# Kernel optimization log

Hardware: AMD Instinct MI355X
Metric: run time of the kernel (lower is better)

The kernel has to match this reference:

```python
import itertools
import jax, jax.numpy as jnp
import numpy as np

N_QUBITS = 8
N_LAYERS = 2
BATCH = 8192
INPUT_DIM = 3072
NUM_CLASSES = 10

_In = np.eye(2, dtype=np.complex64)
_Xn = np.array([[0, 1], [1, 0]], dtype=np.complex64)
_Yn = np.array([[0, -1j], [1j, 0]], dtype=np.complex64)
_Zn = np.array([[1, 0], [0, -1]], dtype=np.complex64)
_P = {"I": _In, "X": _Xn, "Y": _Yn, "Z": _Zn}
_XX = jnp.asarray(np.kron(_Xn, _Xn))
_YY = jnp.asarray(np.kron(_Yn, _Yn))
_ZZ = jnp.asarray(np.kron(_Zn, _Zn))
_I4 = jnp.eye(4, dtype=jnp.complex64)
# 2-qubit Pauli words in PennyLane ArbitraryUnitary order: IX, IY, IZ, XI, ..., ZZ
_WORDS = jnp.asarray(np.stack([np.kron(_P[a], _P[b]) for a, b in itertools.product("IXYZ", repeat=2)][1:]))


def apply_gate(state, U, wires):
    """Apply a 2^k x 2^k gate U to the given wires of a (2,)*n statevector."""
    n = state.ndim
    k = len(wires)
    U = U.reshape((2,) * (2 * k)).astype(state.dtype)
    state = jnp.tensordot(U, state, axes=(list(range(k, 2 * k)), list(wires)))
    rest = [a for a in range(n) if a not in wires]
    perm = [0] * n
    for i, a in enumerate(wires):
        perm[a] = i
    for j, a in enumerate(rest):
        perm[a] = k + j
    return jnp.transpose(state, perm)


def u3_mat(t, p, d):
    ct, st = jnp.cos(t / 2).astype(jnp.complex64), jnp.sin(t / 2).astype(jnp.complex64)
    r0 = jnp.stack([ct, -jnp.exp(1j * d) * st])
    r1 = jnp.stack([jnp.exp(1j * p) * st, jnp.exp(1j * (p + d)) * ct])
    return jnp.stack([r0, r1])


def ry_mat(t):
    c, s = jnp.cos(t / 2), jnp.sin(t / 2)
    return jnp.stack([jnp.stack([c, -s]), jnp.stack([s, c])]).astype(jnp.complex64)


def ising_mat(phi, pauli2):
    # exp(-i phi/2 P) for two-qubit Pauli word P (P^2 = I)
    return jnp.cos(phi / 2) * _I4 - 1j * jnp.sin(phi / 2) * pauli2


def circuit(conv_w, pool_w, last_w, feats):
    state = jnp.zeros((2,) * N_QUBITS, jnp.complex64).at[(0,) * N_QUBITS].set(1.0)
    # AngleEmbedding with RY rotations
    for w in range(N_QUBITS):
        state = apply_gate(state, ry_mat(feats[w]), (w,))
    wires = list(range(N_QUBITS))
    for layer in range(N_LAYERS):
        cw = conv_w[layer]
        nw = len(wires)
        for p in (0, 1):
            for idx in range(nw - 1):
                if idx % 2 == p:
                    a, b = wires[idx], wires[idx + 1]
                    state = apply_gate(state, u3_mat(cw[idx, 0], cw[idx, 1], cw[idx, 2]), (a,))
                    state = apply_gate(state, u3_mat(cw[idx + 1, 3], cw[idx + 1, 4], cw[idx + 1, 5]), (b,))
                    state = apply_gate(state, ising_mat(cw[idx, 6], _ZZ), (a, b))
                    state = apply_gate(state, ising_mat(cw[idx, 7], _YY), (a, b))
                    state = apply_gate(state, ising_mat(cw[idx, 8], _XX), (a, b))
                    state = apply_gate(state, u3_mat(cw[idx, 9], cw[idx, 10], cw[idx, 11]), (a,))
                    state = apply_gate(state, u3_mat(cw[idx + 1, 12], cw[idx + 1, 13], cw[idx + 1, 14]), (b,))
        # Pooling: mid-circuit measure + conditional U3 == (deferred measurement)
        pw = pool_w[layer]
        for idx in range(1, nw, 2):
            u = u3_mat(pw[idx // 2, 0], pw[idx // 2, 1], pw[idx // 2, 2])
            cu = jnp.zeros((4, 4), jnp.complex64).at[0, 0].set(1.0).at[1, 1].set(1.0).at[2:, 2:].set(u)
            state = apply_gate(state, cu, (wires[idx], wires[idx - 1]))
        wires = wires[::2]
    # ArbitraryUnitary on remaining 2 wires: product of 15 PauliRot gates
    for k in range(15):
        mat = jnp.cos(last_w[k] / 2) * _I4 - 1j * jnp.sin(last_w[k] / 2) * _WORDS[k]
        state = apply_gate(state, mat, tuple(wires))
    probs = state.real ** 2 + state.imag ** 2
    z = jnp.sum(probs, axis=tuple(range(1, N_QUBITS)))  # (2,)
    return z[0] - z[1]


def setup_inputs() -> dict:
    key = jax.random.key(0)
    ks = jax.random.split(key, 8)
    return {
        "x": jax.random.normal(ks[0], (BATCH, INPUT_DIM), jnp.float32),
        "fc_w": jax.random.normal(ks[1], (N_QUBITS, INPUT_DIM), jnp.float32) * 0.02,
        "fc_b": jnp.zeros((N_QUBITS,), jnp.float32),
        "conv_params": jax.random.normal(ks[2], (N_LAYERS, N_QUBITS, 15), jnp.float32),
        "pool_params": jax.random.normal(ks[3], (N_LAYERS, N_QUBITS // 2, 3), jnp.float32),
        "last_params": jax.random.normal(ks[4], (15,), jnp.float32),
        "out_w": jax.random.normal(ks[5], (NUM_CLASSES, 1), jnp.float32),
        "out_b": jnp.zeros((NUM_CLASSES,), jnp.float32),
    }


def reference(x, fc_w, fc_b, conv_params, pool_params, last_params, out_w, out_b):
    feats = jnp.tanh(x.reshape(x.shape[0], -1) @ fc_w.T + fc_b)  # (B, n_qubits)
    qvals = jax.vmap(lambda f: circuit(conv_params, pool_params, last_params, f))(feats)
    logits = qvals[:, None].astype(x.dtype) @ out_w.T + out_b  # (B, num_classes)
    return logits
```

## Files before the change

kernel.cpp:

```cpp
#include <hip/hip_runtime.h>
#include <math.h>

__constant__ int G_ORD[17] = {0,1,2,3,4,5,6, 10,11,12,13, 7,8,9, 14,15, 16};
__constant__ int G_WA[17]  = {0,2,4,6,1,3,5, 1,3,5,7, 0,4,2, 2,6, 0};
__constant__ int G_WB[17]  = {1,3,5,7,2,4,6, 0,2,4,6, 2,6,4, 0,4, 4};
__constant__ int CDESC[10][3] = {{0,0,1},{0,2,3},{0,4,5},{0,6,7},{0,1,2},{0,3,4},{0,5,6},
                                 {1,0,1},{1,2,3},{1,1,2}};
__constant__ int PDESC[6][2] = {{0,0},{0,1},{0,2},{0,3},{1,0},{1,1}};
__constant__ float2 PMAT[4][4] = {
  {{1.f,0.f},{0.f,0.f},{0.f,0.f},{1.f,0.f}},
  {{0.f,0.f},{1.f,0.f},{1.f,0.f},{0.f,0.f}},
  {{0.f,0.f},{0.f,-1.f},{0.f,1.f},{0.f,0.f}},
  {{1.f,0.f},{0.f,0.f},{0.f,0.f},{-1.f,0.f}}};

__device__ __forceinline__ float2 cmul(float2 a, float2 b){
  return make_float2(a.x*b.x - a.y*b.y, a.x*b.y + a.y*b.x);
}
__device__ __forceinline__ float2 cadd(float2 a, float2 b){
  return make_float2(a.x+b.x, a.y+b.y);
}

__device__ void u3m(float t, float p, float d, float2* u){
  float ct = cosf(0.5f*t), st = sinf(0.5f*t);
  u[0] = make_float2(ct, 0.f);
  u[1] = make_float2(-cosf(d)*st, -sinf(d)*st);
  u[2] = make_float2(cosf(p)*st,  sinf(p)*st);
  u[3] = make_float2(cosf(p+d)*ct, sinf(p+d)*ct);
}

__device__ void kron2(const float2* A, const float2* B, float2* M){
  #pragma unroll
  for (int ia=0; ia<2; ia++)
    #pragma unroll
    for (int ib=0; ib<2; ib++)
      #pragma unroll
      for (int ja=0; ja<2; ja++)
        #pragma unroll
        for (int jb=0; jb<2; jb++)
          M[(ia*2+ib)*4 + (ja*2+jb)] = cmul(A[ia*2+ja], B[ib*2+jb]);
}

__device__ void mul44(const float2* A, const float2* B, float2* C){
  #pragma unroll
  for (int r=0;r<4;r++)
    #pragma unroll
    for (int c=0;c<4;c++){
      float2 s = make_float2(0.f,0.f);
      #pragma unroll
      for (int k=0;k<4;k++) s = cadd(s, cmul(A[r*4+k], B[k*4+c]));
      C[r*4+c] = s;
    }
}

__device__ void rotword(float phi, int qa, int qb, float2* R){
  float ch = cosf(0.5f*phi), sh = sinf(0.5f*phi);
  float2 W[16];
  kron2(PMAT[qa], PMAT[qb], W);
  #pragma unroll
  for (int i=0;i<16;i++) R[i] = make_float2(sh*W[i].y, -sh*W[i].x);
  #pragma unroll
  for (int d=0;d<4;d++) R[d*4+d].x += ch;
}

__global__ __launch_bounds__(64) void build_gates_kernel(
    const float* __restrict__ conv, const float* __restrict__ pool,
    const float* __restrict__ last, float* __restrict__ gates){
  int t = threadIdx.x;
  float2 M[16], T[16], R[16];
  if (t < 10){
    int layer = CDESC[t][0], ra = CDESC[t][1], rb = CDESC[t][2];
    const float* cw = conv + layer*120;
    int bA = ra*15, bB = rb*15;
    float2 A1[4], B1[4], A2[4], B2[4], K[16];
    u3m(cw[bA+0], cw[bA+1], cw[bA+2], A1);
    u3m(cw[bB+3], cw[bB+4], cw[bB+5], B1);
    kron2(A1, B1, M);
    rotword(cw[bA+6], 3, 3, R); mul44(R, M, T);
    rotword(cw[bA+7], 2, 2, R); mul44(R, T, M);
    rotword(cw[bA+8], 1, 1, R); mul44(R, M, T);
    u3m(cw[bA+9],  cw[bA+10], cw[bA+11], A2);
    u3m(cw[bB+12], cw[bB+13], cw[bB+14], B2);
    kron2(A2, B2, K); mul44(K, T, M);
  } else if (t < 16){
    int layer = PDESC[t-10][0], h = PDESC[t-10][1];
    const float* pw = pool + layer*12 + h*3;
    float2 u[4];
    u3m(pw[0], pw[1], pw[2], u);
    #pragma unroll
    for (int i=0;i<16;i++) M[i] = make_float2(0.f,0.f);
    M[0]  = make_float2(1.f,0.f);
    M[5]  = make_float2(1.f,0.f);
    M[10] = u[0]; M[11] = u[1]; M[14] = u[2]; M[15] = u[3];
  } else if (t == 16){
    #pragma unroll
    for (int i=0;i<16;i++) M[i] = make_float2((i%5==0)?1.f:0.f, 0.f);
    for (int k=0;k<15;k++){
      int w = k+1;
      rotword(last[k], w>>2, w&3, R);
      mul44(R, M, T);
      #pragma unroll
      for (int i=0;i<16;i++) M[i] = T[i];
    }
  }
  if (t < 17){
    float2* dst = (float2*)(gates + t*32);
    #pragma unroll
    for (int i=0;i<16;i++) dst[i] = M[i];
  }
}

__global__ __launch_bounds__(64) void build_u_kernel(
    const float* __restrict__ gates, float2* __restrict__ U){
  __shared__ float2 st[256];
  int lane = threadIdx.x, col = blockIdx.x;
  #pragma unroll
  for (int k=lane; k<256; k+=64) st[k] = make_float2(k==col ? 1.f : 0.f, 0.f);
  __syncthreads();
  for (int g=0; g<17; g++){
    int slot = G_ORD[g];
    const float2* gm = (const float2*)(gates + slot*32);
    float2 m[16];
    #pragma unroll
    for (int i=0;i<16;i++) m[i] = gm[i];
    int pa = 7 - G_WA[g], pb = 7 - G_WB[g];
    int plo = pa < pb ? pa : pb, phi_ = pa < pb ? pb : pa;
    int mm = lane;
    int t1   = ((mm >> plo) << (plo+1)) | (mm & ((1<<plo)-1));
    int base = ((t1 >> phi_) << (phi_+1)) | (t1 & ((1<<phi_)-1));
    int ba = 1<<pa, bb = 1<<pb;
    int i0 = base, i1 = base|bb, i2 = base|ba, i3 = base|ba|bb;
    float2 s0 = st[i0], s1 = st[i1], s2 = st[i2], s3 = st[i3];
    float2 n0 = cadd(cadd(cmul(m[0], s0), cmul(m[1], s1)), cadd(cmul(m[2], s2), cmul(m[3], s3)));
    float2 n1 = cadd(cadd(cmul(m[4], s0), cmul(m[5], s1)), cadd(cmul(m[6], s2), cmul(m[7], s3)));
    float2 n2 = cadd(cadd(cmul(m[8], s0), cmul(m[9], s1)), cadd(cmul(m[10],s2), cmul(m[11],s3)));
    float2 n3 = cadd(cadd(cmul(m[12],s0), cmul(m[13],s1)), cadd(cmul(m[14],s2), cmul(m[15],s3)));
    st[i0] = n0; st[i1] = n1; st[i2] = n2; st[i3] = n3;
    __syncthreads();
  }
  #pragma unroll
  for (int k=lane; k<256; k+=64) U[k*256 + col] = st[k];
}

__global__ __launch_bounds__(256) void build_a_kernel(
    const float2* __restrict__ U, float* __restrict__ A){
  int j = threadIdx.x, i0 = blockIdx.x*2;
  float a0=0.f, a1=0.f;
  #pragma unroll 8
  for (int k=0; k<256; k++){
    float2 uj = U[k*256 + j];
    float2 u0 = U[k*256 + i0+0];
    float2 u1 = U[k*256 + i0+1];
    float sgn = (k < 128) ? 1.f : -1.f;
    a0 += sgn*(u0.x*uj.x + u0.y*uj.y);
    a1 += sgn*(u1.x*uj.x + u1.y*uj.y);
  }
  A[(i0+0)*256 + j] = a0;
  A[(i0+1)*256 + j] = a1;
}

__global__ __launch_bounds__(256) void feats_kernel(
    const float* __restrict__ x, const float* __restrict__ fcw,
    const float* __restrict__ fcb, float* __restrict__ feats){
  __shared__ float red[128*68];
  int t = threadIdx.x, lane = t & 63, wv = t >> 6;
  int r0 = blockIdx.x * 16;
  int rw = r0 + wv*4;
  const float4* x4 = (const float4*)x;
  const float4* w4 = (const float4*)fcw;
  float acc[4][8];
  #pragma unroll
  for (int r=0;r<4;r++)
    #pragma unroll
    for (int o=0;o<8;o++) acc[r][o] = 0.f;
  for (int p=0; p<12; p++){
    float4 wf[8];
    #pragma unroll
    for (int o=0;o<8;o++) wf[o] = w4[o*768 + p*64 + lane];
    #pragma unroll
    for (int r=0;r<4;r++){
      float4 xv = x4[(size_t)(rw+r)*768 + p*64 + lane];
      #pragma unroll
      for (int o=0;o<8;o++){
        acc[r][o] += xv.x*wf[o].x + xv.y*wf[o].y + xv.z*wf[o].z + xv.w*wf[o].w;
      }
    }
  }
  #pragma unroll
  for (int r=0;r<4;r++)
    #pragma unroll
    for (int o=0;o<8;o++)
      red[((wv*4+r)*8 + o)*68 + lane] = acc[r][o];
  __syncthreads();
  if (t < 128){
    const float4* rp = (const float4*)(red + t*68);
    float4 s4 = make_float4(0.f,0.f,0.f,0.f);
    #pragma unroll
    for (int i=0;i<16;i++){
      float4 v = rp[i];
      s4.x += v.x; s4.y += v.y; s4.z += v.z; s4.w += v.w;
    }
    float s = s4.x + s4.y + s4.z + s4.w + fcb[t & 7];
    feats[(r0 + (t>>3))*8 + (t&7)] = tanhf(s);
  }
}

__global__ __launch_bounds__(256) void qform_kernel(
    const float* __restrict__ Ag, const float* __restrict__ feats,
    const float* __restrict__ outw, const float* __restrict__ outb,
    float* __restrict__ out){
  __shared__ float As[32*256];
  __shared__ float ps[16*256];
  int t = threadIdx.x;
  int r0 = blockIdx.x * 16;
  {
    int row = t >> 4, i1 = t & 15;
    const float* f = feats + (r0 + row)*8;
    float c[8], s[8];
    #pragma unroll
    for (int w=0; w<8; w++){
      float a = 0.5f*f[w];
      __sincosf(a, &s[w], &c[w]);
    }
    float Hv = (i1&8 ? s[0]:c[0]) * (i1&4 ? s[1]:c[1])
             * (i1&2 ? s[2]:c[2]) * (i1&1 ? s[3]:c[3]);
    float l2[2], l4[4], l8[8], L[16];
    l2[0]=c[4]; l2[1]=s[4];
    #pragma unroll
    for (int a=0;a<2;a++){ l4[a*2]=l2[a]*c[5]; l4[a*2+1]=l2[a]*s[5]; }
    #pragma unroll
    for (int a=0;a<4;a++){ l8[a*2]=l4[a]*c[6]; l8[a*2+1]=l4[a]*s[6]; }
    #pragma unroll
    for (int a=0;a<8;a++){ L[a*2]=l8[a]*c[7]; L[a*2+1]=l8[a]*s[7]; }
    float* dst = ps + row*256 + i1*16;
    #pragma unroll
    for (int j=0;j<16;j++) dst[j] = Hv*L[j];
  }
  int wv = t >> 6, jb = t & 63;
  const float4* As4 = (const float4*)As;
  const float4* ps4 = (const float4*)ps;
  float4 acc4[4];
  #pragma unroll
  for (int r=0;r<4;r++) acc4[r] = make_float4(0.f,0.f,0.f,0.f);
  for (int chunk=0; chunk<8; chunk++){
    __syncthreads();
    #pragma unroll
    for (int pass=0; pass<8; pass++){
      int kk = pass*4 + wv;
      *(float4*)(As + kk*256 + jb*4) =
        *(const float4*)(Ag + (chunk*32 + kk)*256 + jb*4);
    }
    __syncthreads();
    #pragma unroll
    for (int kk4=0; kk4<8; kk4++){
      float4 av0 = As4[(kk4*4+0)*64 + jb];
      float4 av1 = As4[(kk4*4+1)*64 + jb];
      float4 av2 = As4[(kk4*4+2)*64 + jb];
      float4 av3 = As4[(kk4*4+3)*64 + jb];
      #pragma unroll
      for (int r=0; r<4; r++){
        float4 pv = ps4[(wv*4+r)*64 + chunk*8 + kk4];
        acc4[r].x += pv.x*av0.x + pv.y*av1.x + pv.z*av2.x + pv.w*av3.x;
        acc4[r].y += pv.x*av0.y + pv.y*av1.y + pv.z*av2.y + pv.w*av3.y;
        acc4[r].z += pv.x*av0.z + pv.y*av1.z + pv.z*av2.z + pv.w*av3.z;
        acc4[r].w += pv.x*av0.w + pv.y*av1.w + pv.z*av2.w + pv.w*av3.w;
      }
    }
  }
  float p[4];
  #pragma unroll
  for (int r=0; r<4; r++){
    float4 psv = ps4[(wv*4+r)*64 + jb];
    float pr = acc4[r].x*psv.x + acc4[r].y*psv.y + acc4[r].z*psv.z + acc4[r].w*psv.w;
    #pragma unroll
    for (int m=1; m<64; m<<=1) pr += __shfl_xor(pr, m, 64);
    p[r] = pr;
  }
  if (jb < 40){
    int ridx = jb / 10, c = jb - ridx*10;
    float q = (ridx==0) ? p[0] : (ridx==1) ? p[1] : (ridx==2) ? p[2] : p[3];
    out[(r0 + wv*4 + ridx)*10 + c] = q*outw[c] + outb[c];
  }
}

extern "C" void kernel_launch(void* const* d_in, const int* in_sizes, int n_in,
                              void* d_out, int out_size, void* d_ws, size_t ws_size,
                              hipStream_t stream) {
  const float* x    = (const float*)d_in[0];
  const float* fcw  = (const float*)d_in[1];
  const float* fcb  = (const float*)d_in[2];
  const float* conv = (const float*)d_in[3];
  const float* pool = (const float*)d_in[4];
  const float* last = (const float*)d_in[5];
  const float* outw = (const float*)d_in[6];
  const float* outb = (const float*)d_in[7];
  float* out = (float*)d_out;

  float* ws = (float*)d_ws;
  float*  gates = ws;
  float2* U     = (float2*)(ws + 1024);
  float*  Am    = ws + 1024 + 131072;
  float*  feats = Am + 65536;

  build_gates_kernel<<<1, 64, 0, stream>>>(conv, pool, last, gates);
  build_u_kernel<<<256, 64, 0, stream>>>(gates, U);
  build_a_kernel<<<128, 256, 0, stream>>>(U, Am);
  feats_kernel<<<512, 256, 0, stream>>>(x, fcw, fcb, feats);
  qform_kernel<<<512, 256, 0, stream>>>(Am, feats, outw, outb, out);
}
```

Baseline: 259.0 us.

## Fuse gate building into U kernel, split A rows, retile quadratic-form kernel

Gate matrix construction moves into every build_u block, held in shared memory, which removes one kernel launch and a global round trip, at the cost of redundant per-block gate computation. build_a now computes one row per block across twice as many blocks. The qform kernel drops to 128 threads, each holding 8 row accumulators, writes ps with float4 stores and stages its outputs through shared memory. Lower occupancy and higher register pressure in qform could offset the gains; the feats loop also gets an unroll hint.

```diff
diff --git a/kernel.cpp b/kernel.cpp
--- a/kernel.cpp
+++ b/kernel.cpp
@@ -62,69 +62,65 @@
   for (int d=0;d<4;d++) R[d*4+d].x += ch;
 }
 
-__global__ __launch_bounds__(64) void build_gates_kernel(
+__global__ __launch_bounds__(64) void build_u_kernel(
     const float* __restrict__ conv, const float* __restrict__ pool,
-    const float* __restrict__ last, float* __restrict__ gates){
-  int t = threadIdx.x;
-  float2 M[16], T[16], R[16];
-  if (t < 10){
-    int layer = CDESC[t][0], ra = CDESC[t][1], rb = CDESC[t][2];
-    const float* cw = conv + layer*120;
-    int bA = ra*15, bB = rb*15;
-    float2 A1[4], B1[4], A2[4], B2[4], K[16];
-    u3m(cw[bA+0], cw[bA+1], cw[bA+2], A1);
-    u3m(cw[bB+3], cw[bB+4], cw[bB+5], B1);
-    kron2(A1, B1, M);
-    rotword(cw[bA+6], 3, 3, R); mul44(R, M, T);
-    rotword(cw[bA+7], 2, 2, R); mul44(R, T, M);
-    rotword(cw[bA+8], 1, 1, R); mul44(R, M, T);
-    u3m(cw[bA+9],  cw[bA+10], cw[bA+11], A2);
-    u3m(cw[bB+12], cw[bB+13], cw[bB+14], B2);
-    kron2(A2, B2, K); mul44(K, T, M);
-  } else if (t < 16){
-    int layer = PDESC[t-10][0], h = PDESC[t-10][1];
-    const float* pw = pool + layer*12 + h*3;
-    float2 u[4];
-    u3m(pw[0], pw[1], pw[2], u);
-    #pragma unroll
-    for (int i=0;i<16;i++) M[i] = make_float2(0.f,0.f);
-    M[0]  = make_float2(1.f,0.f);
-    M[5]  = make_float2(1.f,0.f);
-    M[10] = u[0]; M[11] = u[1]; M[14] = u[2]; M[15] = u[3];
-  } else if (t == 16){
-    #pragma unroll
-    for (int i=0;i<16;i++) M[i] = make_float2((i%5==0)?1.f:0.f, 0.f);
-    for (int k=0;k<15;k++){
-      int w = k+1;
-      rotword(last[k], w>>2, w&3, R);
-      mul44(R, M, T);
-      #pragma unroll
-      for (int i=0;i<16;i++) M[i] = T[i];
-    }
-  }
-  if (t < 17){
-    float2* dst = (float2*)(gates + t*32);
-    #pragma unroll
-    for (int i=0;i<16;i++) dst[i] = M[i];
-  }
-}
-
-__global__ __launch_bounds__(64) void build_u_kernel(
-    const float* __restrict__ gates, float2* __restrict__ U){
+    const float* __restrict__ last, float2* __restrict__ U){
+  __shared__ float2 gl[17][16];
   __shared__ float2 st[256];
-  int lane = threadIdx.x, col = blockIdx.x;
-  #pragma unroll
-  for (int k=lane; k<256; k+=64) st[k] = make_float2(k==col ? 1.f : 0.f, 0.f);
+  int t = threadIdx.x, col = blockIdx.x;
+  {
+    float2 M[16], T[16], R[16];
+    if (t < 10){
+      int layer = CDESC[t][0], ra = CDESC[t][1], rb = CDESC[t][2];
+      const float* cw = conv + layer*120;
+      int bA = ra*15, bB = rb*15;
+      float2 A1[4], B1[4], A2[4], B2[4], K[16];
+      u3m(cw[bA+0], cw[bA+1], cw[bA+2], A1);
+      u3m(cw[bB+3], cw[bB+4], cw[bB+5], B1);
+      kron2(A1, B1, M);
+      rotword(cw[bA+6], 3, 3, R); mul44(R, M, T);
+      rotword(cw[bA+7], 2, 2, R); mul44(R, T, M);
+      rotword(cw[bA+8], 1, 1, R); mul44(R, M, T);
+      u3m(cw[bA+9],  cw[bA+10], cw[bA+11], A2);
+      u3m(cw[bB+12], cw[bB+13], cw[bB+14], B2);
+      kron2(A2, B2, K); mul44(K, T, M);
+    } else if (t < 16){
+      int layer = PDESC[t-10][0], h = PDESC[t-10][1];
+      const float* pw = pool + layer*12 + h*3;
+      float2 u[4];
+      u3m(pw[0], pw[1], pw[2], u);
+      #pragma unroll
+      for (int i=0;i<16;i++) M[i] = make_float2(0.f,0.f);
+      M[0]  = make_float2(1.f,0.f);
+      M[5]  = make_float2(1.f,0.f);
+      M[10] = u[0]; M[11] = u[1]; M[14] = u[2]; M[15] = u[3];
+    } else if (t == 16){
+      #pragma unroll
+      for (int i=0;i<16;i++) M[i] = make_float2((i%5==0)?1.f:0.f, 0.f);
+      for (int k=0;k<15;k++){
+        int w = k+1;
+        rotword(last[k], w>>2, w&3, R);
+        mul44(R, M, T);
+        #pragma unroll
+        for (int i=0;i<16;i++) M[i] = T[i];
+      }
+    }
+    if (t < 17){
+      #pragma unroll
+      for (int i=0;i<16;i++) gl[t][i] = M[i];
+    }
+  }
+  #pragma unroll
+  for (int k=t; k<256; k+=64) st[k] = make_float2(k==col ? 1.f : 0.f, 0.f);
   __syncthreads();
   for (int g=0; g<17; g++){
     int slot = G_ORD[g];
-    const float2* gm = (const float2*)(gates + slot*32);
     float2 m[16];
     #pragma unroll
-    for (int i=0;i<16;i++) m[i] = gm[i];
+    for (int i=0;i<16;i++) m[i] = gl[slot][i];
     int pa = 7 - G_WA[g], pb = 7 - G_WB[g];
     int plo = pa < pb ? pa : pb, phi_ = pa < pb ? pb : pa;
-    int mm = lane;
+    int mm = t;
     int t1   = ((mm >> plo) << (plo+1)) | (mm & ((1<<plo)-1));
     int base = ((t1 >> phi_) << (phi_+1)) | (t1 & ((1<<phi_)-1));
     int ba = 1<<pa, bb = 1<<pb;
@@ -138,24 +134,21 @@
     __syncthreads();
   }
   #pragma unroll
-  for (int k=lane; k<256; k+=64) U[k*256 + col] = st[k];
+  for (int k=t; k<256; k+=64) U[k*256 + col] = st[k];
 }
 
 __global__ __launch_bounds__(256) void build_a_kernel(
     const float2* __restrict__ U, float* __restrict__ A){
-  int j = threadIdx.x, i0 = blockIdx.x*2;
-  float a0=0.f, a1=0.f;
+  int j = threadIdx.x, i = blockIdx.x;
+  float a0 = 0.f;
   #pragma unroll 8
   for (int k=0; k<256; k++){
     float2 uj = U[k*256 + j];
-    float2 u0 = U[k*256 + i0+0];
-    float2 u1 = U[k*256 + i0+1];
+    float2 ui = U[k*256 + i];
     float sgn = (k < 128) ? 1.f : -1.f;
-    a0 += sgn*(u0.x*uj.x + u0.y*uj.y);
-    a1 += sgn*(u1.x*uj.x + u1.y*uj.y);
-  }
-  A[(i0+0)*256 + j] = a0;
-  A[(i0+1)*256 + j] = a1;
+    a0 += sgn*(ui.x*uj.x + ui.y*uj.y);
+  }
+  A[i*256 + j] = a0;
 }
 
 __global__ __launch_bounds__(256) void feats_kernel(
@@ -172,6 +165,7 @@
   for (int r=0;r<4;r++)
     #pragma unroll
     for (int o=0;o<8;o++) acc[r][o] = 0.f;
+  #pragma unroll 2
   for (int p=0; p<12; p++){
     float4 wf[8];
     #pragma unroll
@@ -204,16 +198,17 @@
   }
 }
 
-__global__ __launch_bounds__(256) void qform_kernel(
+__global__ __launch_bounds__(128) void qform_kernel(
     const float* __restrict__ Ag, const float* __restrict__ feats,
     const float* __restrict__ outw, const float* __restrict__ outb,
     float* __restrict__ out){
   __shared__ float As[32*256];
   __shared__ float ps[16*256];
+  __shared__ float qv[16];
   int t = threadIdx.x;
   int r0 = blockIdx.x * 16;
   {
-    int row = t >> 4, i1 = t & 15;
+    int row = t >> 3, sub = t & 7;
     const float* f = feats + (r0 + row)*8;
     float c[8], s[8];
     #pragma unroll
@@ -221,8 +216,8 @@
       float a = 0.5f*f[w];
       __sincosf(a, &s[w], &c[w]);
     }
-    float Hv = (i1&8 ? s[0]:c[0]) * (i1&4 ? s[1]:c[1])
-             * (i1&2 ? s[2]:c[2]) * (i1&1 ? s[3]:c[3]);
+    float hr = (sub&4 ? s[1]:c[1]) * (sub&2 ? s[2]:c[2]) * (sub&1 ? s[3]:c[3]);
+    float Hv_a = c[0]*hr, Hv_b = s[0]*hr;
     float l2[2], l4[4], l8[8], L[16];
     l2[0]=c[4]; l2[1]=s[4];
     #pragma unroll
@@ -231,34 +226,39 @@
     for (int a=0;a<4;a++){ l8[a*2]=l4[a]*c[6]; l8[a*2+1]=l4[a]*s[6]; }
     #pragma unroll
     for (int a=0;a<8;a++){ L[a*2]=l8[a]*c[7]; L[a*2+1]=l8[a]*s[7]; }
-    float* dst = ps + row*256 + i1*16;
-    #pragma unroll
-    for (int j=0;j<16;j++) dst[j] = Hv*L[j];
+    float4* da = (float4*)(ps + row*256 + sub*16);
+    float4* db = (float4*)(ps + row*256 + (sub+8)*16);
+    #pragma unroll
+    for (int qd=0; qd<4; qd++){
+      da[qd] = make_float4(Hv_a*L[qd*4+0], Hv_a*L[qd*4+1], Hv_a*L[qd*4+2], Hv_a*L[qd*4+3]);
+      db[qd] = make_float4(Hv_b*L[qd*4+0], Hv_b*L[qd*4+1], Hv_b*L[qd*4+2], Hv_b*L[qd*4+3]);
+    }
   }
   int wv = t >> 6, jb = t & 63;
   const float4* As4 = (const float4*)As;
   const float4* ps4 = (const float4*)ps;
-  float4 acc4[4];
-  #pragma unroll
-  for (int r=0;r<4;r++) acc4[r] = make_float4(0.f,0.f,0.f,0.f);
+  const float4* Ag4 = (const float4*)Ag;
+  float4 acc4[8];
+  #pragma unroll
+  for (int r=0;r<8;r++) acc4[r] = make_float4(0.f,0.f,0.f,0.f);
   for (int chunk=0; chunk<8; chunk++){
     __syncthreads();
     #pragma unroll
-    for (int pass=0; pass<8; pass++){
-      int kk = pass*4 + wv;
-      *(float4*)(As + kk*256 + jb*4) =
-        *(const float4*)(Ag + (chunk*32 + kk)*256 + jb*4);
+    for (int pass=0; pass<16; pass++){
+      int kk = pass*2 + wv;
+      As4[0];
+      *(float4*)(As + kk*256 + jb*4) = Ag4[(chunk*32 + kk)*64 + jb];
     }
     __syncthreads();
-    #pragma unroll
-    for (int kk4=0; kk4<8; kk4++){
-      float4 av0 = As4[(kk4*4+0)*64 + jb];
-      float4 av1 = As4[(kk4*4+1)*64 + jb];
-      float4 av2 = As4[(kk4*4+2)*64 + jb];
-      float4 av3 = As4[(kk4*4+3)*64 + jb];
-      #pragma unroll
-      for (int r=0; r<4; r++){
-        float4 pv = ps4[(wv*4+r)*64 + chunk*8 + kk4];
+    #pragma unroll 2
+    for (int kq=0; kq<8; kq++){
+      float4 av0 = As4[(kq*4+0)*64 + jb];
+      float4 av1 = As4[(kq*4+1)*64 + jb];
+      float4 av2 = As4[(kq*4+2)*64 + jb];
+      float4 av3 = As4[(kq*4+3)*64 + jb];
+      #pragma unroll
+      for (int r=0; r<8; r++){
+        float4 pv = ps4[(wv*8+r)*64 + chunk*8 + kq];
         acc4[r].x += pv.x*av0.x + pv.y*av1.x + pv.z*av2.x + pv.w*av3.x;
         acc4[r].y += pv.x*av0.y + pv.y*av1.y + pv.z*av2.y + pv.w*av3.y;
         acc4[r].z += pv.x*av0.z + pv.y*av1.z + pv.z*av2.z + pv.w*av3.z;
@@ -266,19 +266,18 @@
       }
     }
   }
-  float p[4];
-  #pragma unroll
-  for (int r=0; r<4; r++){
-    float4 psv = ps4[(wv*4+r)*64 + jb];
+  #pragma unroll
+  for (int r=0; r<8; r++){
+    float4 psv = ps4[(wv*8+r)*64 + jb];
     float pr = acc4[r].x*psv.x + acc4[r].y*psv.y + acc4[r].z*psv.z + acc4[r].w*psv.w;
     #pragma unroll
     for (int m=1; m<64; m<<=1) pr += __shfl_xor(pr, m, 64);
-    p[r] = pr;
-  }
-  if (jb < 40){
-    int ridx = jb / 10, c = jb - ridx*10;
-    float q = (ridx==0) ? p[0] : (ridx==1) ? p[1] : (ridx==2) ? p[2] : p[3];
-    out[(r0 + wv*4 + ridx)*10 + c] = q*outw[c] + outb[c];
+    if (jb == 0) qv[wv*8 + r] = pr;
+  }
+  __syncthreads();
+  for (int u=t; u<160; u+=128){
+    int row = u/10, c = u - row*10;
+    out[(r0 + row)*10 + c] = qv[row]*outw[c] + outb[c];
   }
 }
 
@@ -296,14 +295,12 @@
   float* out = (float*)d_out;
 
   float* ws = (float*)d_ws;
-  float*  gates = ws;
-  float2* U     = (float2*)(ws + 1024);
-  float*  Am    = ws + 1024 + 131072;
+  float2* U     = (float2*)ws;
+  float*  Am    = ws + 131072;
   float*  feats = Am + 65536;
 
-  build_gates_kernel<<<1, 64, 0, stream>>>(conv, pool, last, gates);
-  build_u_kernel<<<256, 64, 0, stream>>>(gates, U);
-  build_a_kernel<<<128, 256, 0, stream>>>(U, Am);
+  build_u_kernel<<<256, 64, 0, stream>>>(conv, pool, last, U);
+  build_a_kernel<<<256, 256, 0, stream>>>(U, Am);
   feats_kernel<<<512, 256, 0, stream>>>(x, fcw, fcb, feats);
-  qform_kernel<<<512, 256, 0, stream>>>(Am, feats, outw, outb, out);
-}
+  qform_kernel<<<512, 128, 0, stream>>>(Am, feats, outw, outb, out);
+}
```

New measurement: 271.1 us. 1.05x slower.
